# Performance work log

Measured on AMD Instinct MI355X. Metric: run time of the kernel, lower is better.

Reference implementation:

```python
import jax, jax.numpy as jnp
import numpy as np

EPS = 1e-5

def mvn(x):
    # per-(N,C) spatial mean/std normalization; torch .var is unbiased (ddof=1)
    mean = jnp.mean(x, axis=(2, 3), keepdims=True)
    var = jnp.var(x, axis=(2, 3), ddof=1, keepdims=True)
    return (x - mean) / jnp.sqrt(var + EPS)

def conv1x1(x, w, b):
    # w: [O, C] (1x1 conv collapsed), x: [B, C, H, W]
    return jnp.einsum('bchw,oc->bohw', x, w) + b[None, :, None, None]

def conv3x3(x, w, b):
    # w: [O, I, 3, 3], VALID padding (snet uses padding=0)
    y = jax.lax.conv_general_dilated(x, w, (1, 1), 'VALID',
                                     dimension_numbers=('NCHW', 'OIHW', 'NCHW'))
    return y + b[None, :, None, None]

def safe_cbrt(x):
    # pow(relu(x), 1/3) with safe gradient at 0 (forward identical)
    pos = x > 0
    return jnp.where(pos, jnp.power(jnp.where(pos, x, 1.0), 1.0 / 3.0), 0.0)

def _forward(content, style, wf_san, bf_san, wg_san, bg_san, wh_san, bh_san,
             wf_mcc, bf_mcc, wg_mcc, bg_mcc, w_fc, b_fc, w_out, b_out,
             wc1, bc1, wc2, bc2, wc3, bc3, ws1, bs1, ws2, bs2, ws3, bs3,
             w_unc, b_unc):
    B, C, H, W = content.shape
    cn = mvn(content)
    sn = mvn(style)

    # --- MCC branch: channel correlation statistic of style ---
    F_Fc = conv1x1(cn, wf_mcc, bf_mcc)                      # [B,C,H,W]
    g = conv1x1(sn, wg_mcc, bg_mcc).reshape(B, C, H * W)    # [B,C,HW]
    FC_S = jnp.sum(g * g, axis=-1) / jnp.sum(g, axis=-1)    # [B,C]
    FC_S = FC_S @ w_fc.T + b_fc                             # Linear
    part1 = F_Fc * FC_S[:, :, None, None]

    # --- WCT-like covariance branch (compressed 32-dim space) ---
    Fs0 = style - jnp.mean(style, axis=(2, 3), keepdims=True)  # nor_mean
    fc_ = conv1x1(jax.nn.relu(conv1x1(jax.nn.relu(conv1x1(cn, wc1, bc1)), wc2, bc2)), wc3, bc3)  # [B,32,H,W]
    fs_ = conv1x1(jax.nn.relu(conv3x3(jax.nn.relu(conv3x3(Fs0, ws1, bs1)), ws2, bs2)), ws3, bs3)  # [B,32,H-4,W-4]
    cdim = fc_.shape[1]
    fs_flat = fs_.reshape(B, cdim, -1)                       # [B,32,hw_s]
    cov = jnp.einsum('bci,bdi->bcd', fs_flat, fs_flat) / fs_flat.shape[2]  # [B,32,32]
    out = jnp.einsum('bcd,bdi->bci', cov, fc_.reshape(B, cdim, H * W)).reshape(B, cdim, H, W)
    part2 = conv1x1(out, w_unc, b_unc)                       # [B,512,H,W]

    # --- SANet-style attention branch ---
    F_s = conv1x1(cn, wf_san, bf_san).reshape(B, C, H * W)
    G_s = conv1x1(sn, wg_san, bg_san).reshape(B, C, H * W)
    H_s = conv1x1(style, wh_san, bh_san).reshape(B, C, H * W)
    S = jax.nn.softmax(jnp.einsum('bci,bcj->bij', F_s, G_s), axis=-1)  # [B,HW,HW]
    part3 = jnp.einsum('bcj,bij->bci', H_s, S).reshape(B, C, H, W)

    p = safe_cbrt(jax.nn.relu(part1 * part2 * part3))
    return conv1x1(p, w_out, b_out) + content


def setup_inputs() -> dict:
    key = jax.random.key(0)
    B, C, H, W = 16, 512, 32, 32
    s = 0.02
    shapes = {
        'content': (B, C, H, W), 'style': (B, C, H, W),
        'wf_san': (C, C), 'bf_san': (C,), 'wg_san': (C, C), 'bg_san': (C,),
        'wh_san': (C, C), 'bh_san': (C,),
        'wf_mcc': (C, C), 'bf_mcc': (C,), 'wg_mcc': (C, C), 'bg_mcc': (C,),
        'w_fc': (C, C), 'b_fc': (C,), 'w_out': (C, C), 'b_out': (C,),
        'wc1': (256, 512), 'bc1': (256,), 'wc2': (128, 256), 'bc2': (128,),
        'wc3': (32, 128), 'bc3': (32,),
        'ws1': (256, 512, 3, 3), 'bs1': (256,), 'ws2': (128, 256, 3, 3), 'bs2': (128,),
        'ws3': (32, 128), 'bs3': (32,),
        'w_unc': (512, 32), 'b_unc': (512,),
    }
    d = {}
    for i, (name, shp) in enumerate(shapes.items()):
        k = jax.random.fold_in(key, i)
        scale = 1.0 if name in ('content', 'style') else s
        d[name] = jax.random.normal(k, shp, dtype=jnp.float32) * scale
    return d


def reference(content, style, wf_san, bf_san, wg_san, bg_san, wh_san, bh_san,
              wf_mcc, bf_mcc, wg_mcc, bg_mcc, w_fc, b_fc, w_out, b_out,
              wc1, bc1, wc2, bc2, wc3, bc3, ws1, bs1, ws2, bs2, ws3, bs3,
              w_unc, b_unc):
    return _forward(content, style, wf_san, bf_san, wg_san, bg_san, wh_san, bh_san,
                    wf_mcc, bf_mcc, wg_mcc, bg_mcc, w_fc, b_fc, w_out, b_out,
                    wc1, bc1, wc2, bc2, wc3, bc3, ws1, bs1, ws2, bs2, ws3, bs3,
                    w_unc, b_unc)
```

## Files before the change

### kernel.cpp

```cpp
#include <hip/hip_runtime.h>
#include <hip/hip_bf16.h>
#include <math.h>


typedef __attribute__((ext_vector_type(8))) short short8;
typedef __attribute__((ext_vector_type(4))) float f32x4;
typedef unsigned short us;
#define MFMA16 __builtin_amdgcn_mfma_f32_16x16x32_bf16

__device__ inline float b2f(us b) { return __uint_as_float(((unsigned)b) << 16); }
__device__ inline us f2b(float f) {
    unsigned u = __float_as_uint(f);
    return (us)((u + 0x7FFFu + ((u >> 16) & 1u)) >> 16);
}

__device__ inline double blockReduceSumD(double v, double* sh) {
    int t = threadIdx.x;
    sh[t] = v; __syncthreads();
    for (int s = blockDim.x >> 1; s > 0; s >>= 1) {
        if (t < s) sh[t] += sh[t + s];
        __syncthreads();
    }
    double r = sh[0]; __syncthreads();
    return r;
}

__global__ __launch_bounds__(256) void stats_k(const float* __restrict__ X,
                                               float* __restrict__ mean,
                                               float* __restrict__ inv, int HW) {
    __shared__ double sh[256];
    int bc = blockIdx.x;
    const float* x = X + (size_t)bc * HW;
    int t = threadIdx.x;
    float v[4];
    double s = 0.0;
    #pragma unroll
    for (int r = 0; r < 4; ++r) { v[r] = x[t + r * 256]; s += (double)v[r]; }
    double tot = blockReduceSumD(s, sh);
    double ss = 0.0;
    #pragma unroll
    for (int r = 0; r < 4; ++r) ss += (double)v[r] * (double)v[r];
    double tot2 = blockReduceSumD(ss, sh);
    if (t == 0) {
        double m = tot / HW;
        double var = (tot2 - tot * tot / HW) / (HW - 1);
        mean[bc] = (float)m;
        inv[bc] = (float)(1.0 / sqrt(var + 1e-5));
    }
}

__global__ __launch_bounds__(256) void trn_k(const float* __restrict__ X,
                                             const float* __restrict__ mean,
                                             const float* __restrict__ inv,
                                             us* __restrict__ Yn, us* __restrict__ Yc,
                                             us* __restrict__ Yr, int C, int HW) {
    __shared__ us Ln[64 * 65];
    __shared__ us Lc[64 * 65];
    __shared__ us Lr[64 * 65];
    int bz = blockIdx.z, c0 = blockIdx.y * 64, h0 = blockIdx.x * 64;
    const float* Xb = X + (size_t)bz * C * HW;
    int t = threadIdx.x;
    int cl = t >> 3, h8 = (t & 7) * 8;
    #pragma unroll
    for (int half = 0; half < 2; ++half) {
        int c = cl + half * 32;
        int gc = c0 + c;
        float m = mean[bz * C + gc], iv = inv[bz * C + gc];
        const float4* s4 = (const float4*)&Xb[(size_t)gc * HW + h0 + h8];
        float4 f0 = s4[0], f1 = s4[1];
        float vv[8] = {f0.x, f0.y, f0.z, f0.w, f1.x, f1.y, f1.z, f1.w};
        #pragma unroll
        for (int i = 0; i < 8; ++i) {
            int li = c * 65 + h8 + i;
            if (Yn) Ln[li] = f2b((vv[i] - m) * iv);
            if (Yc) Lc[li] = f2b(vv[i] - m);
            if (Yr) Lr[li] = f2b(vv[i]);
        }
    }
    __syncthreads();
    int hl = t >> 3, c8 = (t & 7) * 8;
    #pragma unroll
    for (int half = 0; half < 2; ++half) {
        int hh = hl + half * 32;
        size_t off = ((size_t)bz * HW + h0 + hh) * (size_t)C + c0 + c8;
        us tmp[8];
        if (Yn) {
            #pragma unroll
            for (int i = 0; i < 8; ++i) tmp[i] = Ln[(c8 + i) * 65 + hh];
            *(uint4*)&Yn[off] = *(const uint4*)tmp;
        }
        if (Yc) {
            #pragma unroll
            for (int i = 0; i < 8; ++i) tmp[i] = Lc[(c8 + i) * 65 + hh];
            *(uint4*)&Yc[off] = *(const uint4*)tmp;
        }
        if (Yr) {
            #pragma unroll
            for (int i = 0; i < 8; ++i) tmp[i] = Lr[(c8 + i) * 65 + hh];
            *(uint4*)&Yr[off] = *(const uint4*)tmp;
        }
    }
}

template <typename TE>
__device__ inline void stage16(const TE* __restrict__ src, bool valid, us* dst) {
    us tmp[16];
    if (valid) {
        if constexpr (sizeof(TE) == 2) {
            uint4 a = ((const uint4*)src)[0], b = ((const uint4*)src)[1];
            *(uint4*)&tmp[0] = a; *(uint4*)&tmp[8] = b;
        } else {
            const float4* s4 = (const float4*)src;
            float4 f0 = s4[0], f1 = s4[1], f2 = s4[2], f3 = s4[3];
            float vv[16] = {f0.x, f0.y, f0.z, f0.w, f1.x, f1.y, f1.z, f1.w,
                            f2.x, f2.y, f2.z, f2.w, f3.x, f3.y, f3.z, f3.w};
            #pragma unroll
            for (int i = 0; i < 16; ++i) tmp[i] = f2b(vv[i]);
        }
    } else {
        #pragma unroll
        for (int i = 0; i < 16; ++i) tmp[i] = 0;
    }
    ((uint4*)dst)[0] = *(uint4*)&tmp[0];
    ((uint4*)dst)[1] = *(uint4*)&tmp[8];
}

template <typename TAel, typename TBel, typename TOUT, int OUTT>
__global__ __launch_bounds__(256) void mf2_k(const TAel* __restrict__ A, long astride, int lda,
                                             const TBel* __restrict__ B, long bstride, int ldb,
                                             const float* __restrict__ bias,
                                             TOUT* __restrict__ Y,
                                             const float* __restrict__ add_src,
                                             int K, int M, int N, int relu) {
    __shared__ us As[128][40];
    __shared__ us Bs[128][40];
    int bz = blockIdx.z;
    int mbase = blockIdx.y * 128, nbase = blockIdx.x * 128;
    const TAel* Ab = A + (size_t)bz * astride;
    const TBel* Bb = B + (size_t)bz * bstride;
    int t = threadIdx.x;
    int row = t & 127, kh = t >> 7;
    int wave = t >> 6, lane = t & 63, lm = lane & 15, q = lane >> 4;
    int mh = (wave >> 1) * 64, nh = (wave & 1) * 64;

    f32x4 acc[4][4];
    #pragma unroll
    for (int i = 0; i < 4; ++i)
        #pragma unroll
        for (int j = 0; j < 4; ++j) acc[i][j] = (f32x4){0.f, 0.f, 0.f, 0.f};

    for (int kb = 0; kb < K; kb += 32) {
        int gm = mbase + row;
        stage16(Ab + (size_t)gm * lda + kb + kh * 16, gm < M, &As[row][kh * 16]);
        int gn = nbase + row;
        stage16(Bb + (size_t)gn * ldb + kb + kh * 16, gn < N, &Bs[row][kh * 16]);
        __syncthreads();
        short8 af[4], bf[4];
        #pragma unroll
        for (int i = 0; i < 4; ++i) af[i] = *(const short8*)&As[mh + i * 16 + lm][q * 8];
        #pragma unroll
        for (int j = 0; j < 4; ++j) bf[j] = *(const short8*)&Bs[nh + j * 16 + lm][q * 8];
        #pragma unroll
        for (int i = 0; i < 4; ++i)
            #pragma unroll
            for (int j = 0; j < 4; ++j)
                acc[i][j] = MFMA16(af[i], bf[j], acc[i][j], 0, 0, 0);
        __syncthreads();
    }

    #pragma unroll
    for (int i = 0; i < 4; ++i) {
        int m0 = mbase + mh + i * 16 + q * 4;
        if (m0 >= M) continue;
        float bv[4];
        #pragma unroll
        for (int r = 0; r < 4; ++r) bv[r] = bias ? bias[m0 + r] : 0.f;
        #pragma unroll
        for (int j = 0; j < 4; ++j) {
            int n = nbase + nh + j * 16 + lm;
            if (n >= N) continue;
            float v[4];
            #pragma unroll
            for (int r = 0; r < 4; ++r) {
                float x = acc[i][j][r] + bv[r];
                if (relu) x = (x > 0.f) ? x : 0.f;
                v[r] = x;
            }
            if (OUTT == 1) {
                size_t off = ((size_t)bz * N + n) * (size_t)M + m0;
                if constexpr (sizeof(TOUT) == 2) {
                    us o4[4];
                    #pragma unroll
                    for (int r = 0; r < 4; ++r) o4[r] = f2b(v[r]);
                    *(uint2*)&Y[off] = *(const uint2*)o4;
                } else {
                    float4 f4 = make_float4(v[0], v[1], v[2], v[3]);
                    *(float4*)&Y[off] = f4;
                }
            } else {
                #pragma unroll
                for (int r = 0; r < 4; ++r) {
                    size_t off = ((size_t)bz * M + m0 + r) * (size_t)N + n;
                    float x = v[r];
                    if (add_src) x += add_src[off];
                    if constexpr (sizeof(TOUT) == 2) Y[off] = f2b(x);
                    else Y[off] = x;
                }
            }
        }
    }
}

__global__ __launch_bounds__(256) void reorder_w3_k(const float* __restrict__ W,
                                                    us* __restrict__ Wr, int O, int Cin) {
    int idx = blockIdx.x * 256 + threadIdx.x;
    int total = 9 * O * Cin;
    if (idx >= total) return;
    int tap = idx / (O * Cin);
    int rem = idx - tap * (O * Cin);
    int o = rem / Cin;
    int c = rem - o * Cin;
    Wr[idx] = f2b(W[((size_t)o * Cin + c) * 9 + tap]);
}

__global__ __launch_bounds__(256) void conv_mf2_k(const us* __restrict__ X, long xbstride,
                                                  const us* __restrict__ Wr,
                                                  const float* __restrict__ bias,
                                                  us* __restrict__ Y, long ybstride,
                                                  int Cin, int O, int IH, int IW,
                                                  int OH, int OW) {
    __shared__ us patch[4 * 36 * 40];
    __shared__ us Ws[9 * 64 * 40];
    int bz = blockIdx.z;
    int obase = blockIdx.y * 64;
    int pyb = blockIdx.x * 2;
    const us* Xb = X + (size_t)bz * xbstride;
    int t = threadIdx.x;
    int wave = t >> 6, lane = t & 63, lm = lane & 15, q = lane >> 4;
    int mh = (wave >> 1) * 32, rw = wave & 1;

    f32x4 acc[2][2];
    #pragma unroll
    for (int i = 0; i < 2; ++i)
        #pragma unroll
        for (int j = 0; j < 2; ++j) acc[i][j] = (f32x4){0.f, 0.f, 0.f, 0.f};

    for (int cb = 0; cb < Cin; cb += 32) {
        __syncthreads();
        for (int i = t; i < 576; i += 256) {
            int p = i >> 2, q8 = (i & 3) * 8;
            int r = p / 36, x = p - r * 36;
            int gy = pyb + r;
            uint4 v = make_uint4(0u, 0u, 0u, 0u);
            if (x < IW && gy < IH)
                v = *(const uint4*)&Xb[((size_t)(gy * IW + x)) * Cin + cb + q8];
            *(uint4*)&patch[p * 40 + q8] = v;
        }
        for (int rowi = t; rowi < 576; rowi += 256) {
            int o_local = rowi & 63, tap = rowi >> 6;
            const us* src = Wr + ((size_t)tap * O + obase + o_local) * Cin + cb;
            uint4 a = ((const uint4*)src)[0], b = ((const uint4*)src)[1];
            uint4 c2 = ((const uint4*)src)[2], d = ((const uint4*)src)[3];
            us* dst = &Ws[rowi * 40];
            ((uint4*)dst)[0] = a; ((uint4*)dst)[1] = b;
            ((uint4*)dst)[2] = c2; ((uint4*)dst)[3] = d;
        }
        __syncthreads();
        #pragma unroll
        for (int tap = 0; tap < 9; ++tap) {
            int ky = tap / 3, kx = tap - ky * 3;
            short8 a0 = *(const short8*)&Ws[(tap * 64 + mh + lm) * 40 + q * 8];
            short8 a1 = *(const short8*)&Ws[(tap * 64 + mh + 16 + lm) * 40 + q * 8];
            int prow = (rw + ky) * 36;
            short8 b0 = *(const short8*)&patch[(prow + lm + kx) * 40 + q * 8];
            short8 b1 = *(const short8*)&patch[(prow + 16 + lm + kx) * 40 + q * 8];
            acc[0][0] = MFMA16(a0, b0, acc[0][0], 0, 0, 0);
            acc[0][1] = MFMA16(a0, b1, acc[0][1], 0, 0, 0);
            acc[1][0] = MFMA16(a1, b0, acc[1][0], 0, 0, 0);
            acc[1][1] = MFMA16(a1, b1, acc[1][1], 0, 0, 0);
        }
    }

    int py = pyb + rw;
    us* Yb = Y + (size_t)bz * ybstride;
    #pragma unroll
    for (int i = 0; i < 2; ++i) {
        int m0 = obase + mh + i * 16 + q * 4;
        #pragma unroll
        for (int j = 0; j < 2; ++j) {
            int px = j * 16 + lm;
            if (px >= OW) continue;
            us o4[4];
            #pragma unroll
            for (int r = 0; r < 4; ++r) {
                float v = acc[i][j][r] + bias[m0 + r];
                v = (v > 0.f) ? v : 0.f;
                o4[r] = f2b(v);
            }
            *(uint2*)&Yb[((size_t)(py * OW + px)) * O + m0] = *(const uint2*)o4;
        }
    }
}

__global__ __launch_bounds__(256) void gemm_k(const float* __restrict__ W,
                                              const float* __restrict__ X,
                                              const float* __restrict__ bias,
                                              float* __restrict__ Y,
                                              int C, int O, int N) {
    int obase = blockIdx.y * 32;
    __shared__ float As[32][33];
    __shared__ float Bs[32][33];
    int t = threadIdx.x;
    int tx = t & 15, ty = t >> 4;
    float acc00 = 0, acc01 = 0, acc10 = 0, acc11 = 0;
    for (int cb = 0; cb < C; cb += 32) {
        int k = t & 31, o0 = t >> 5;
        #pragma unroll
        for (int r = 0; r < 4; ++r) {
            int ol = o0 + r * 8;
            As[k][ol] = W[(size_t)(obase + ol) * C + cb + k];
        }
        int n0 = t & 31, k0 = t >> 5;
        #pragma unroll
        for (int r = 0; r < 4; ++r) {
            int k2 = k0 + r * 8;
            Bs[k2][n0] = (n0 < N) ? X[(size_t)(cb + k2) * N + n0] : 0.f;
        }
        __syncthreads();
        #pragma unroll
        for (int k2 = 0; k2 < 32; ++k2) {
            float a0 = As[k2][ty], a1 = As[k2][ty + 16];
            float b0 = Bs[k2][tx], b1 = Bs[k2][tx + 16];
            acc00 += a0 * b0; acc01 += a0 * b1;
            acc10 += a1 * b0; acc11 += a1 * b1;
        }
        __syncthreads();
    }
    float accs[2][2] = {{acc00, acc01}, {acc10, acc11}};
    #pragma unroll
    for (int i = 0; i < 2; ++i) {
        int o = obase + ty + i * 16;
        float bv = bias[o];
        #pragma unroll
        for (int j = 0; j < 2; ++j) {
            int n = tx + j * 16;
            if (n < N) Y[(size_t)o * N + n] = accs[i][j] + bv;
        }
    }
}

__global__ __launch_bounds__(256) void fcs2_k(const us* __restrict__ g,
                                              const float* __restrict__ bg,
                                              float* __restrict__ fcs,
                                              int HW, int B, int C) {
    __shared__ double sh[256];
    int bc = blockIdx.x;
    int b = bc / C, c = bc - b * C;
    const us* x = g + (size_t)bc * HW;
    int t = threadIdx.x;
    uint2 v = *(const uint2*)&x[t * 4];
    us u[4]; *(uint2*)u = v;
    double ss = 0.0;
    #pragma unroll
    for (int i = 0; i < 4; ++i) { double gv = (double)b2f(u[i]); ss += gv * gv; }
    double tss = blockReduceSumD(ss, sh);
    if (t == 0) fcs[(size_t)c * B + b] = (float)(tss / ((double)HW * (double)bg[c]));
}

__global__ __launch_bounds__(256) void softmax_k(const float* __restrict__ S,
                                                 us* __restrict__ P) {
    __shared__ float sh[256];
    size_t row = blockIdx.x;
    const float* r = S + row * 1024;
    us* po = P + row * 1024;
    int t = threadIdx.x;
    float v[4];
    float m = -INFINITY;
    #pragma unroll
    for (int i = 0; i < 4; ++i) { v[i] = r[t + i * 256]; m = fmaxf(m, v[i]); }
    sh[t] = m; __syncthreads();
    for (int s = 128; s > 0; s >>= 1) { if (t < s) sh[t] = fmaxf(sh[t], sh[t + s]); __syncthreads(); }
    m = sh[0]; __syncthreads();
    float sum = 0;
    #pragma unroll
    for (int i = 0; i < 4; ++i) { v[i] = expf(v[i] - m); sum += v[i]; }
    sh[t] = sum; __syncthreads();
    for (int s = 128; s > 0; s >>= 1) { if (t < s) sh[t] += sh[t + s]; __syncthreads(); }
    float inv = 1.f / sh[0]; __syncthreads();
    #pragma unroll
    for (int i = 0; i < 4; ++i) po[t + i * 256] = f2b(v[i] * inv);
}

__global__ __launch_bounds__(256) void cov2_k(const float* __restrict__ fs,
                                              float* __restrict__ cov, int Cd, int M) {
    __shared__ float Ls[196 * 36];
    int bb = blockIdx.x;
    int t = threadIdx.x;
    const float* p = fs + (size_t)bb * M * Cd;
    int c = t >> 3, d0 = (t & 7) * 4;
    float a0 = 0.f, a1 = 0.f, a2 = 0.f, a3 = 0.f;
    for (int ch = 0; ch < 4; ++ch) {
        __syncthreads();
        for (int i = t; i < 1568; i += 256) {
            int rowi = i >> 3, c4 = (i & 7) * 4;
            float4 v = *(const float4*)&p[(size_t)(ch * 196 + rowi) * Cd + c4];
            *(float4*)&Ls[rowi * 36 + c4] = v;
        }
        __syncthreads();
        for (int i = 0; i < 196; ++i) {
            float a = Ls[i * 36 + c];
            a0 += a * Ls[i * 36 + d0 + 0];
            a1 += a * Ls[i * 36 + d0 + 1];
            a2 += a * Ls[i * 36 + d0 + 2];
            a3 += a * Ls[i * 36 + d0 + 3];
        }
    }
    float invM = 1.f / (float)M;
    size_t base = ((size_t)bb * Cd + c) * Cd + d0;
    cov[base + 0] = a0 * invM;
    cov[base + 1] = a1 * invM;
    cov[base + 2] = a2 * invM;
    cov[base + 3] = a3 * invM;
}

__global__ __launch_bounds__(256) void fuse_k(const us* __restrict__ ffc,
                                              const float* __restrict__ fc2t,
                                              const us* __restrict__ p2,
                                              const us* __restrict__ p3,
                                              us* __restrict__ out, int B, int C, int HW) {
    size_t idx = (size_t)blockIdx.x * 256 + threadIdx.x;
    size_t total = (size_t)B * C * HW;
    if (idx >= total) return;
    int c = (int)(idx & (size_t)(C - 1));
    int b = (int)(idx / ((size_t)C * HW));
    float part1 = b2f(ffc[idx]) * fc2t[(size_t)c * B + b];
    float v = part1 * b2f(p2[idx]) * b2f(p3[idx]);
    v = (v > 0.f) ? v : 0.f;
    out[idx] = f2b(cbrtf(v));
}

extern "C" void kernel_launch(void* const* d_in, const int* in_sizes, int n_in,
                              void* d_out, int out_size, void* d_ws, size_t ws_size,
                              hipStream_t stream) {
    typedef const float* fp;
    fp content = (fp)d_in[0];
    fp style   = (fp)d_in[1];
    fp wf_san = (fp)d_in[2],  bf_san = (fp)d_in[3];
    fp wg_san = (fp)d_in[4],  bg_san = (fp)d_in[5];
    fp wh_san = (fp)d_in[6],  bh_san = (fp)d_in[7];
    fp wf_mcc = (fp)d_in[8],  bf_mcc = (fp)d_in[9];
    fp wg_mcc = (fp)d_in[10], bg_mcc = (fp)d_in[11];
    fp w_fc   = (fp)d_in[12], b_fc   = (fp)d_in[13];
    fp w_out  = (fp)d_in[14], b_out  = (fp)d_in[15];
    fp wc1 = (fp)d_in[16], bc1 = (fp)d_in[17];
    fp wc2 = (fp)d_in[18], bc2 = (fp)d_in[19];
    fp wc3 = (fp)d_in[20], bc3 = (fp)d_in[21];
    fp ws1 = (fp)d_in[22], bs1 = (fp)d_in[23];
    fp ws2 = (fp)d_in[24], bs2 = (fp)d_in[25];
    fp ws3 = (fp)d_in[26], bs3 = (fp)d_in[27];
    fp w_unc = (fp)d_in[28], b_unc = (fp)d_in[29];

    const int B = 16, C = 512, HW = 1024;
    const size_t NE = (size_t)B * C * HW;
    const long TOK = (long)C * HW;
    char* base = (char*)d_ws;
    const size_t SL = 16777216;

    us* gbuf  = (us*)(base + 0 * SL);
    float* Sbuf  = (float*)(base + 0 * SL);
    us* fs0T  = (us*)(base + 3 * SL);
    us* cnT   = (us*)(base + 4 * SL);
    us* snT   = (us*)(base + 5 * SL);
    us* Pb    = (us*)(base + 4 * SL);
    us* styleT = (us*)(base + 6 * SL);
    us* ffcb  = (us*)(base + 7 * SL);
    us* Fsb   = (us*)(base + 8 * SL);
    us* Gsb   = (us*)(base + 9 * SL);
    us* part2 = (us*)(base + 10 * SL);
    us* t1 = (us*)(base + 11 * SL);
    us* t2 = (us*)(base + 11 * SL + 8388608);
    us* s1 = (us*)(base + 12 * SL);
    us* s2 = (us*)(base + 12 * SL + 7372800);
    us* part3 = Fsb;
    us* Hco   = Gsb;
    us* pbuf  = ffcb;

    char* misc = base + 13 * SL;
    us* Wr1 = (us*)(misc);
    us* Wr2 = (us*)(misc + 2359296);
    float* fc_c  = (float*)(misc + 2949120);
    float* fs_c  = (float*)(misc + 5046272);
    float* out32 = (float*)(misc + 6651904);
    float* fcs   = (float*)(misc + 8749056);
    float* fc2t  = (float*)(misc + 8781824);
    float* cov   = (float*)(misc + 8814592);
    float* meanC = (float*)(misc + 8880128);
    float* invC  = (float*)(misc + 8912896);
    float* meanS = (float*)(misc + 8945664);
    float* invS  = (float*)(misc + 8978432);

    reorder_w3_k<<<4608, 256, 0, stream>>>(ws1, Wr1, 256, 512);
    reorder_w3_k<<<1152, 256, 0, stream>>>(ws2, Wr2, 128, 256);

    stats_k<<<B * C, 256, 0, stream>>>(content, meanC, invC, HW);
    stats_k<<<B * C, 256, 0, stream>>>(style, meanS, invS, HW);
    trn_k<<<dim3(16, 8, 16), 256, 0, stream>>>(content, meanC, invC, cnT, nullptr, nullptr, C, HW);
    trn_k<<<dim3(16, 8, 16), 256, 0, stream>>>(style, meanS, invS, snT, fs0T, styleT, C, HW);

    mf2_k<float, us, us, 0><<<dim3(8, 4, 16), 256, 0, stream>>>(
        wg_mcc, 0, 512, snT, TOK, 512, bg_mcc, gbuf, nullptr, 512, 512, 1024, 0);
    fcs2_k<<<B * C, 256, 0, stream>>>(gbuf, bg_mcc, fcs, HW, B, C);
    gemm_k<<<dim3(1, 16, 1), 256, 0, stream>>>(w_fc, fcs, b_fc, fc2t, 512, 512, 16);

    mf2_k<float, us, us, 1><<<dim3(8, 4, 16), 256, 0, stream>>>(
        wf_mcc, 0, 512, cnT, TOK, 512, bf_mcc, ffcb, nullptr, 512, 512, 1024, 0);

    mf2_k<float, us, us, 1><<<dim3(8, 2, 16), 256, 0, stream>>>(
        wc1, 0, 512, cnT, TOK, 512, bc1, t1, nullptr, 512, 256, 1024, 1);
    mf2_k<float, us, us, 1><<<dim3(8, 1, 16), 256, 0, stream>>>(
        wc2, 0, 256, t1, (long)1024 * 256, 256, bc2, t2, nullptr, 256, 128, 1024, 1);
    mf2_k<float, us, float, 1><<<dim3(8, 1, 16), 256, 0, stream>>>(
        wc3, 0, 128, t2, (long)1024 * 128, 128, bc3, fc_c, nullptr, 128, 32, 1024, 0);

    conv_mf2_k<<<dim3(15, 4, 16), 256, 0, stream>>>(fs0T, TOK, Wr1, bs1,
                                                    s1, (long)900 * 256, 512, 256, 32, 32, 30, 30);
    conv_mf2_k<<<dim3(14, 2, 16), 256, 0, stream>>>(s1, (long)900 * 256, Wr2, bs2,
                                                    s2, (long)784 * 128, 256, 128, 30, 30, 28, 28);
    mf2_k<float, us, float, 1><<<dim3(7, 1, 16), 256, 0, stream>>>(
        ws3, 0, 128, s2, (long)784 * 128, 128, bs3, fs_c, nullptr, 128, 32, 784, 0);

    cov2_k<<<B, 256, 0, stream>>>(fs_c, cov, 32, 784);
    mf2_k<float, float, float, 1><<<dim3(8, 1, 16), 256, 0, stream>>>(
        cov, 1024, 32, fc_c, (long)1024 * 32, 32, nullptr, out32, nullptr, 32, 32, 1024, 0);
    mf2_k<float, float, us, 1><<<dim3(8, 4, 16), 256, 0, stream>>>(
        w_unc, 0, 32, out32, (long)1024 * 32, 32, b_unc, part2, nullptr, 32, 512, 1024, 0);

    mf2_k<float, us, us, 1><<<dim3(8, 4, 16), 256, 0, stream>>>(
        wf_san, 0, 512, cnT, TOK, 512, bf_san, Fsb, nullptr, 512, 512, 1024, 0);
    mf2_k<float, us, us, 1><<<dim3(8, 4, 16), 256, 0, stream>>>(
        wg_san, 0, 512, snT, TOK, 512, bg_san, Gsb, nullptr, 512, 512, 1024, 0);

    mf2_k<us, us, float, 0><<<dim3(8, 8, 16), 256, 0, stream>>>(
        Fsb, TOK, 512, Gsb, TOK, 512, nullptr, Sbuf, nullptr, 512, 1024, 1024, 0);
    softmax_k<<<B * HW, 256, 0, stream>>>(Sbuf, Pb);

    mf2_k<float, us, us, 0><<<dim3(8, 4, 16), 256, 0, stream>>>(
        wh_san, 0, 512, styleT, TOK, 512, bh_san, Hco, nullptr, 512, 512, 1024, 0);

    mf2_k<us, us, us, 0><<<dim3(4, 8, 16), 256, 0, stream>>>(
        Pb, (long)1024 * 1024, 1024, Hco, TOK, 1024, nullptr, part3, nullptr, 1024, 1024, 512, 0);

    fuse_k<<<(unsigned)((NE + 255) / 256), 256, 0, stream>>>(ffcb, fc2t, part2, part3, pbuf, B, C, HW);

    mf2_k<float, us, float, 0><<<dim3(8, 4, 16), 256, 0, stream>>>(
        w_out, 0, 512, pbuf, TOK, 512, b_out, (float*)d_out, content, 512, 512, 1024, 0);
}
```

Baseline: 923.5 us.

## Pre-swizzle 3x3 conv weights into MFMA fragment order and process more rows per block

Conv weights are reordered once into the exact per-lane MFMA A-fragment layout, so the conv kernel reads A operands directly from global memory instead of staging a 64x9x32 weight tile through shared memory each K-step. The first 3x3 conv also computes four output rows per block (PR=2), reusing each weight fragment across two row pairs and halving the grid along y. This removes the LDS weight copy and one shared-memory footprint at the cost of uncached-in-LDS global weight loads per wave and more accumulator registers.

```diff
diff --git a/kernel.cpp b/kernel.cpp
--- a/kernel.cpp
+++ b/kernel.cpp
@@ -211,93 +211,108 @@
     }
 }
 
-__global__ __launch_bounds__(256) void reorder_w3_k(const float* __restrict__ W,
-                                                    us* __restrict__ Wr, int O, int Cin) {
+__global__ __launch_bounds__(256) void reorder_wf_k(const float* __restrict__ W,
+                                                    us* __restrict__ Wf, int O, int Cin) {
     int idx = blockIdx.x * 256 + threadIdx.x;
-    int total = 9 * O * Cin;
+    int OT = O >> 6, KB = Cin >> 5;
+    int total = OT * KB * 9 * 4 * 64;
     if (idx >= total) return;
-    int tap = idx / (O * Cin);
-    int rem = idx - tap * (O * Cin);
-    int o = rem / Cin;
-    int c = rem - o * Cin;
-    Wr[idx] = f2b(W[((size_t)o * Cin + c) * 9 + tap]);
-}
-
-__global__ __launch_bounds__(256) void conv_mf2_k(const us* __restrict__ X, long xbstride,
-                                                  const us* __restrict__ Wr,
+    int lane = idx & 63;
+    int f = idx >> 6;
+    int i = f & 1, half = (f >> 1) & 1;
+    int tf = f >> 2;
+    int tap = tf % 9;
+    int rest = tf / 9;
+    int kb = rest % KB, ot = rest / KB;
+    int o = ot * 64 + half * 32 + i * 16 + (lane & 15);
+    int cb = kb * 32 + (lane >> 4) * 8;
+    us v[8];
+    #pragma unroll
+    for (int e = 0; e < 8; ++e)
+        v[e] = f2b(W[((size_t)o * Cin + cb + e) * 9 + tap]);
+    *(uint4*)&Wf[(size_t)idx * 8] = *(const uint4*)v;
+}
+
+template <int PR>
+__global__ __launch_bounds__(256) void conv_mf3_k(const us* __restrict__ X, long xbstride,
+                                                  const us* __restrict__ Wf,
                                                   const float* __restrict__ bias,
                                                   us* __restrict__ Y, long ybstride,
                                                   int Cin, int O, int IH, int IW,
                                                   int OH, int OW) {
-    __shared__ us patch[4 * 36 * 40];
-    __shared__ us Ws[9 * 64 * 40];
+    __shared__ us patch[(2 * PR + 2) * 36 * 40];
     int bz = blockIdx.z;
     int obase = blockIdx.y * 64;
-    int pyb = blockIdx.x * 2;
+    int pyb = blockIdx.x * (2 * PR);
     const us* Xb = X + (size_t)bz * xbstride;
     int t = threadIdx.x;
     int wave = t >> 6, lane = t & 63, lm = lane & 15, q = lane >> 4;
-    int mh = (wave >> 1) * 32, rw = wave & 1;
-
-    f32x4 acc[2][2];
-    #pragma unroll
-    for (int i = 0; i < 2; ++i)
-        #pragma unroll
-        for (int j = 0; j < 2; ++j) acc[i][j] = (f32x4){0.f, 0.f, 0.f, 0.f};
-
-    for (int cb = 0; cb < Cin; cb += 32) {
-        __syncthreads();
-        for (int i = t; i < 576; i += 256) {
+    int half = wave >> 1, rw = wave & 1;
+    int KB = Cin >> 5;
+    const us* Wb = Wf + (size_t)(obase >> 6) * KB * 9 * 2048;
+
+    f32x4 acc[PR][2][2];
+    #pragma unroll
+    for (int pr = 0; pr < PR; ++pr)
+        #pragma unroll
+        for (int i = 0; i < 2; ++i)
+            #pragma unroll
+            for (int j = 0; j < 2; ++j) acc[pr][i][j] = (f32x4){0.f, 0.f, 0.f, 0.f};
+
+    const int ITEMS = (2 * PR + 2) * 36 * 4;
+    for (int kb = 0; kb < KB; ++kb) {
+        __syncthreads();
+        for (int i = t; i < ITEMS; i += 256) {
             int p = i >> 2, q8 = (i & 3) * 8;
             int r = p / 36, x = p - r * 36;
             int gy = pyb + r;
             uint4 v = make_uint4(0u, 0u, 0u, 0u);
             if (x < IW && gy < IH)
-                v = *(const uint4*)&Xb[((size_t)(gy * IW + x)) * Cin + cb + q8];
+                v = *(const uint4*)&Xb[((size_t)(gy * IW + x)) * Cin + kb * 32 + q8];
             *(uint4*)&patch[p * 40 + q8] = v;
         }
-        for (int rowi = t; rowi < 576; rowi += 256) {
-            int o_local = rowi & 63, tap = rowi >> 6;
-            const us* src = Wr + ((size_t)tap * O + obase + o_local) * Cin + cb;
-            uint4 a = ((const uint4*)src)[0], b = ((const uint4*)src)[1];
-            uint4 c2 = ((const uint4*)src)[2], d = ((const uint4*)src)[3];
-            us* dst = &Ws[rowi * 40];
-            ((uint4*)dst)[0] = a; ((uint4*)dst)[1] = b;
-            ((uint4*)dst)[2] = c2; ((uint4*)dst)[3] = d;
-        }
-        __syncthreads();
+        __syncthreads();
+        const us* Wk = Wb + (size_t)kb * 9 * 2048;
         #pragma unroll
         for (int tap = 0; tap < 9; ++tap) {
             int ky = tap / 3, kx = tap - ky * 3;
-            short8 a0 = *(const short8*)&Ws[(tap * 64 + mh + lm) * 40 + q * 8];
-            short8 a1 = *(const short8*)&Ws[(tap * 64 + mh + 16 + lm) * 40 + q * 8];
-            int prow = (rw + ky) * 36;
-            short8 b0 = *(const short8*)&patch[(prow + lm + kx) * 40 + q * 8];
-            short8 b1 = *(const short8*)&patch[(prow + 16 + lm + kx) * 40 + q * 8];
-            acc[0][0] = MFMA16(a0, b0, acc[0][0], 0, 0, 0);
-            acc[0][1] = MFMA16(a0, b1, acc[0][1], 0, 0, 0);
-            acc[1][0] = MFMA16(a1, b0, acc[1][0], 0, 0, 0);
-            acc[1][1] = MFMA16(a1, b1, acc[1][1], 0, 0, 0);
-        }
-    }
-
-    int py = pyb + rw;
+            const us* wt = Wk + tap * 2048 + half * 1024;
+            short8 a0 = *(const short8*)&wt[lane * 8];
+            short8 a1 = *(const short8*)&wt[512 + lane * 8];
+            #pragma unroll
+            for (int pr = 0; pr < PR; ++pr) {
+                int prow = (pr * 2 + rw + ky) * 36;
+                short8 b0 = *(const short8*)&patch[(prow + lm + kx) * 40 + q * 8];
+                short8 b1 = *(const short8*)&patch[(prow + 16 + lm + kx) * 40 + q * 8];
+                acc[pr][0][0] = MFMA16(a0, b0, acc[pr][0][0], 0, 0, 0);
+                acc[pr][0][1] = MFMA16(a0, b1, acc[pr][0][1], 0, 0, 0);
+                acc[pr][1][0] = MFMA16(a1, b0, acc[pr][1][0], 0, 0, 0);
+                acc[pr][1][1] = MFMA16(a1, b1, acc[pr][1][1], 0, 0, 0);
+            }
+        }
+    }
+
     us* Yb = Y + (size_t)bz * ybstride;
     #pragma unroll
-    for (int i = 0; i < 2; ++i) {
-        int m0 = obase + mh + i * 16 + q * 4;
-        #pragma unroll
-        for (int j = 0; j < 2; ++j) {
-            int px = j * 16 + lm;
-            if (px >= OW) continue;
-            us o4[4];
-            #pragma unroll
-            for (int r = 0; r < 4; ++r) {
-                float v = acc[i][j][r] + bias[m0 + r];
-                v = (v > 0.f) ? v : 0.f;
-                o4[r] = f2b(v);
+    for (int pr = 0; pr < PR; ++pr) {
+        int py = pyb + pr * 2 + rw;
+        if (py >= OH) continue;
+        #pragma unroll
+        for (int i = 0; i < 2; ++i) {
+            int m0 = obase + half * 32 + i * 16 + q * 4;
+            #pragma unroll
+            for (int j = 0; j < 2; ++j) {
+                int px = j * 16 + lm;
+                if (px >= OW) continue;
+                us o4[4];
+                #pragma unroll
+                for (int r = 0; r < 4; ++r) {
+                    float v = acc[pr][i][j][r] + bias[m0 + r];
+                    v = (v > 0.f) ? v : 0.f;
+                    o4[r] = f2b(v);
+                }
+                *(uint2*)&Yb[((size_t)(py * OW + px)) * O + m0] = *(const uint2*)o4;
             }
-            *(uint2*)&Yb[((size_t)(py * OW + px)) * O + m0] = *(const uint2*)o4;
         }
     }
 }
@@ -499,8 +514,8 @@
     float* meanS = (float*)(misc + 8945664);
     float* invS  = (float*)(misc + 8978432);
 
-    reorder_w3_k<<<4608, 256, 0, stream>>>(ws1, Wr1, 256, 512);
-    reorder_w3_k<<<1152, 256, 0, stream>>>(ws2, Wr2, 128, 256);
+    reorder_wf_k<<<576, 256, 0, stream>>>(ws1, Wr1, 256, 512);
+    reorder_wf_k<<<72, 256, 0, stream>>>(ws2, Wr2, 128, 256);
 
     stats_k<<<B * C, 256, 0, stream>>>(content, meanC, invC, HW);
     stats_k<<<B * C, 256, 0, stream>>>(style, meanS, invS, HW);
@@ -522,10 +537,10 @@
     mf2_k<float, us, float, 1><<<dim3(8, 1, 16), 256, 0, stream>>>(
         wc3, 0, 128, t2, (long)1024 * 128, 128, bc3, fc_c, nullptr, 128, 32, 1024, 0);
 
-    conv_mf2_k<<<dim3(15, 4, 16), 256, 0, stream>>>(fs0T, TOK, Wr1, bs1,
-                                                    s1, (long)900 * 256, 512, 256, 32, 32, 30, 30);
-    conv_mf2_k<<<dim3(14, 2, 16), 256, 0, stream>>>(s1, (long)900 * 256, Wr2, bs2,
-                                                    s2, (long)784 * 128, 256, 128, 30, 30, 28, 28);
+    conv_mf3_k<2><<<dim3(8, 4, 16), 256, 0, stream>>>(fs0T, TOK, Wr1, bs1,
+                                                      s1, (long)900 * 256, 512, 256, 32, 32, 30, 30);
+    conv_mf3_k<1><<<dim3(14, 2, 16), 256, 0, stream>>>(s1, (long)900 * 256, Wr2, bs2,
+                                                       s2, (long)784 * 128, 256, 128, 30, 30, 28, 28);
     mf2_k<float, us, float, 1><<<dim3(7, 1, 16), 256, 0, stream>>>(
         ws3, 0, 128, s2, (long)784 * 128, 128, bs3, fs_c, nullptr, 128, 32, 784, 0);
 
```

Measured after the change: 898.5 us. 1.03x faster.
